# Kernel tuning notes

Measured on AMD Instinct MI355X. Metric: run time of the kernel, lower is better.

The kernel has to match this reference:

```python
import jax, jax.numpy as jnp
import numpy as np

N = 10000
E = 80000


def gat_layer(x, src, dst, W, a_src, a_dst, b):
    # x: [N, Fin], W: [Fin, Fout]
    xw = x @ W                              # [N, Fout]
    al_src = xw @ a_src                     # [N]
    al_dst = xw @ a_dst                     # [N]
    e = jax.nn.leaky_relu(al_src[src] + al_dst[dst], 0.2)  # [E+N]
    m = jax.lax.stop_gradient(jax.ops.segment_max(e, dst, num_segments=N))
    ex = jnp.exp(e - m[dst])
    denom = jax.ops.segment_sum(ex, dst, num_segments=N)
    alpha = ex / (denom[dst] + 1e-16)       # PyG softmax eps
    out = jax.ops.segment_sum(alpha[:, None] * xw[src], dst, num_segments=N)
    return out + b


def setup_inputs() -> dict:
    key = jax.random.key(0)
    ks = jax.random.split(key, 12)
    x = jax.random.normal(ks[0], (N, 256), dtype=jnp.float32)
    edge_index = jax.random.randint(ks[1], (2, E), 0, N, dtype=jnp.int64)
    def glorot(k, fi, fo):
        return jax.random.normal(k, (fi, fo), jnp.float32) * jnp.sqrt(2.0 / (fi + fo))
    W1 = glorot(ks[2], 256, 2048)
    W2 = glorot(ks[3], 2048, 2048)
    W3 = glorot(ks[4], 2048, 1024)
    a1s = jax.random.normal(ks[5], (2048,), jnp.float32) * 0.05
    a1d = jax.random.normal(ks[6], (2048,), jnp.float32) * 0.05
    a2s = jax.random.normal(ks[7], (2048,), jnp.float32) * 0.05
    a2d = jax.random.normal(ks[8], (2048,), jnp.float32) * 0.05
    a3s = jax.random.normal(ks[9], (1024,), jnp.float32) * 0.05
    a3d = jax.random.normal(ks[10], (1024,), jnp.float32) * 0.05
    b1 = jnp.zeros((2048,), jnp.float32)
    b2 = jnp.zeros((2048,), jnp.float32)
    b3 = jnp.zeros((1024,), jnp.float32)
    return {"x": x, "edge_index": edge_index, "W1": W1, "W2": W2, "W3": W3,
            "a1s": a1s, "a1d": a1d, "a2s": a2s, "a2d": a2d, "a3s": a3s, "a3d": a3d,
            "b1": b1, "b2": b2, "b3": b3}


def reference(x, edge_index, W1, W2, W3, a1s, a1d, a2s, a2d, a3s, a3d, b1, b2, b3):
    # add self loops (PyG GATConv default add_self_loops=True)
    loop = jnp.arange(N, dtype=edge_index.dtype)
    src = jnp.concatenate([edge_index[0], loop])
    dst = jnp.concatenate([edge_index[1], loop])
    h = jax.nn.relu(gat_layer(x, src, dst, W1, a1s, a1d, b1))
    h = jax.nn.relu(gat_layer(h, src, dst, W2, a2s, a2d, b2))
    h = jax.nn.relu(gat_layer(h, src, dst, W3, a3s, a3d, b3))
    # F.normalize(dim=1), eps=1e-12
    norm = jnp.linalg.norm(h, axis=1, keepdims=True)
    return h / jnp.maximum(norm, 1e-12)
```

## Files before the change

kernel.cpp:

```cpp
#include <hip/hip_runtime.h>
#include <hip/hip_bf16.h>
#include <math.h>


typedef __attribute__((ext_vector_type(8))) short short8;
typedef __attribute__((ext_vector_type(4))) float f32x4;

#define GLOAD_LDS16(g, l)                                            \
  __builtin_amdgcn_global_load_lds(                                  \
      (const __attribute__((address_space(1))) void*)(g),            \
      (__attribute__((address_space(3))) void*)(l), 16, 0, 0)

__device__ __forceinline__ float bf16_to_f32(ushort u) {
  return __uint_as_float(((unsigned int)u) << 16);
}

__device__ __forceinline__ float block_reduce_sum_bcast(float v) {
#pragma unroll
  for (int off = 32; off > 0; off >>= 1) v += __shfl_down(v, off, 64);
  __shared__ float tmp[4];
  __shared__ float res;
  int lane = threadIdx.x & 63, w = threadIdx.x >> 6;
  if (lane == 0) tmp[w] = v;
  __syncthreads();
  if (threadIdx.x == 0) res = tmp[0] + tmp[1] + tmp[2] + tmp[3];
  __syncthreads();
  float out = res;
  __syncthreads();
  return out;
}

__device__ __forceinline__ float block_reduce_max_bcast(float v) {
#pragma unroll
  for (int off = 32; off > 0; off >>= 1) v = fmaxf(v, __shfl_down(v, off, 64));
  __shared__ float tmpm[4];
  __shared__ float resm;
  int lane = threadIdx.x & 63, w = threadIdx.x >> 6;
  if (lane == 0) tmpm[w] = v;
  __syncthreads();
  if (threadIdx.x == 0) resm = fmaxf(fmaxf(tmpm[0], tmpm[1]), fmaxf(tmpm[2], tmpm[3]));
  __syncthreads();
  float out = resm;
  __syncthreads();
  return out;
}

__global__ void detect_kernel(const int* __restrict__ ei32, int* __restrict__ flag) {
  __shared__ int cnt;
  if (threadIdx.x == 0) cnt = 0;
  __syncthreads();
  int zeros = 0;
  for (int i = threadIdx.x; i < 1024; i += 256) {
    if (ei32[2 * i + 1] == 0) zeros++;
  }
  atomicAdd(&cnt, zeros);
  __syncthreads();
  if (threadIdx.x == 0) *flag = (cnt > 900) ? 1 : 0;
}

__global__ void convert_kernel(const void* __restrict__ ei, const int* __restrict__ flag,
                               int E, int* __restrict__ src, int* __restrict__ dst) {
  int i = blockIdx.x * blockDim.x + threadIdx.x;
  if (i >= E) return;
  if (*flag) {
    const long long* p = (const long long*)ei;
    src[i] = (int)p[i];
    dst[i] = (int)p[E + i];
  } else {
    const int* p = (const int*)ei;
    src[i] = p[i];
    dst[i] = p[E + i];
  }
}

__global__ __launch_bounds__(256) void convert_f32_bf16(const float* __restrict__ in,
                                                        __hip_bfloat16* __restrict__ out,
                                                        int n) {
  int i = blockIdx.x * blockDim.x + threadIdx.x;
  if (i < n) out[i] = __float2bfloat16(in[i]);
}

__global__ __launch_bounds__(256) void transpose_w(const float* __restrict__ W,
                                                   __hip_bfloat16* __restrict__ Wt,
                                                   int K, int Nout) {
  __shared__ float t[32][33];
  int tx = threadIdx.x & 31, ty = threadIdx.x >> 5;
  int n0 = blockIdx.x * 32, k0 = blockIdx.y * 32;
#pragma unroll
  for (int i = 0; i < 4; ++i) {
    int k = k0 + ty + i * 8;
    t[ty + i * 8][tx] = W[(size_t)k * Nout + n0 + tx];
  }
  __syncthreads();
#pragma unroll
  for (int i = 0; i < 4; ++i) {
    int n = n0 + ty + i * 8;
    Wt[(size_t)n * K + k0 + tx] = __float2bfloat16(t[tx][ty + i * 8]);
  }
}

template <bool BF16OUT>
__global__ __launch_bounds__(512, 2) void gemm256(const ushort* __restrict__ A,
                                                  const ushort* __restrict__ Bt,
                                                  void* __restrict__ C,
                                                  int M, int K, int Nout) {
  extern __shared__ ushort lds[];
  const int tid = threadIdx.x;
  const int l = tid & 63, w = tid >> 6;
  const int wm = w >> 2, wn = w & 3;
  const int l15 = l & 15, lhi = l >> 4;
  const int row0 = blockIdx.y * 256, col0 = blockIdx.x * 256;
  const int c8sw = (l & 3) ^ (((l >> 5) & 1) << 1);
  const int lrow = l >> 2;
  const int chsw = lhi ^ (((l15 >> 3) & 1) << 1);
  const int rd_off = l15 * 32 + chsw * 8;

  const ushort* ga[2][2];
  const ushort* gb[2][2];
  const int sA0 = wm * 8 + wn * 2;
  const int sB0 = (wn >> 1) * 8 + (wm * 2 + (wn & 1)) * 2;
#pragma unroll
  for (int sc = 0; sc < 2; ++sc) {
#pragma unroll
    for (int j = 0; j < 2; ++j) {
      int ar = min(row0 + (sA0 + j) * 16 + lrow, M - 1);
      ga[sc][j] = A + (size_t)ar * K + sc * 32 + c8sw * 8;
      gb[sc][j] = Bt + (size_t)(col0 + (sB0 + j) * 16 + lrow) * K + sc * 32 + c8sw * 8;
    }
  }

#define STAGE_A(nb, kn, sc)                                                       \
  do {                                                                            \
    GLOAD_LDS16(ga[sc][0] + (kn), &lds[(nb)*32768 + ((sA0 + 0) * 2 + (sc)) * 512]); \
    GLOAD_LDS16(ga[sc][1] + (kn), &lds[(nb)*32768 + ((sA0 + 1) * 2 + (sc)) * 512]); \
  } while (0)
#define STAGE_B(nb, kn, sc)                                                       \
  do {                                                                            \
    GLOAD_LDS16(gb[sc][0] + (kn), &lds[(nb)*32768 + 16384 + ((sB0 + 0) * 2 + (sc)) * 512]); \
    GLOAD_LDS16(gb[sc][1] + (kn), &lds[(nb)*32768 + 16384 + ((sB0 + 1) * 2 + (sc)) * 512]); \
  } while (0)

  f32x4 acc[8][4] = {};

#define PHASE(cur, mh, kk, STAGE_STMT)                                            \
  do {                                                                            \
    short8 af[4], bf[4];                                                          \
    const ushort* Ab = &lds[(cur)*32768];                                         \
    const ushort* Bb = &lds[(cur)*32768 + 16384];                                 \
    _Pragma("unroll") for (int m = 0; m < 4; ++m)                                 \
        af[m] = *(const short8*)(Ab + ((wm * 8 + (mh)*4 + m) * 2 + (kk)) * 512 + rd_off); \
    _Pragma("unroll") for (int n = 0; n < 4; ++n)                                 \
        bf[n] = *(const short8*)(Bb + ((wn * 4 + n) * 2 + (kk)) * 512 + rd_off);  \
    STAGE_STMT;                                                                   \
    asm volatile("s_waitcnt vmcnt(4)" ::: "memory");                              \
    __builtin_amdgcn_s_barrier();                                                 \
    __builtin_amdgcn_s_setprio(1);                                                \
    _Pragma("unroll") for (int m = 0; m < 4; ++m)                                 \
        _Pragma("unroll") for (int n = 0; n < 4; ++n)                             \
            acc[(mh)*4 + m][n] = __builtin_amdgcn_mfma_f32_16x16x32_bf16(         \
                af[m], bf[n], acc[(mh)*4 + m][n], 0, 0, 0);                       \
    __builtin_amdgcn_s_setprio(0);                                                \
    __builtin_amdgcn_s_barrier();                                                 \
  } while (0)

  STAGE_A(0, 0, 0);
  STAGE_B(0, 0, 0);
  STAGE_A(0, 0, 1);
  STAGE_B(0, 0, 1);
  asm volatile("s_waitcnt vmcnt(0)" ::: "memory");
  __builtin_amdgcn_s_barrier();

  const int nt = K >> 6;
  int cur = 0;
  for (int t = 0; t < nt; ++t) {
    const int kn = (t + 1) << 6;
    const bool pf = (t + 1) < nt;
    const int nb = cur ^ 1;
    PHASE(cur, 0, 0, if (pf) STAGE_A(nb, kn, 0));
    PHASE(cur, 1, 0, if (pf) STAGE_B(nb, kn, 0));
    PHASE(cur, 0, 1, if (pf) STAGE_A(nb, kn, 1));
    PHASE(cur, 1, 1, if (pf) STAGE_B(nb, kn, 1));
    cur ^= 1;
  }

#pragma unroll
  for (int mi = 0; mi < 8; ++mi) {
#pragma unroll
    for (int v = 0; v < 4; ++v) {
      int r = row0 + wm * 128 + mi * 16 + lhi * 4 + v;
      if (r < M) {
#pragma unroll
        for (int n = 0; n < 4; ++n) {
          size_t idx = (size_t)r * Nout + col0 + wn * 64 + n * 16 + l15;
          if (BF16OUT)
            ((__hip_bfloat16*)C)[idx] = __float2bfloat16(acc[mi][n][v]);
          else
            ((float*)C)[idx] = acc[mi][n][v];
        }
      }
    }
  }
#undef PHASE
#undef STAGE_A
#undef STAGE_B
}

template <bool BF16IN>
__global__ __launch_bounds__(256) void compute_al(const void* __restrict__ xw,
                                                  const float* __restrict__ a_s,
                                                  const float* __restrict__ a_d,
                                                  float* __restrict__ als,
                                                  float* __restrict__ ald, int F) {
  int n = blockIdx.x;
  float s1 = 0.f, s2 = 0.f;
  if (BF16IN) {
    const ushort* row = (const ushort*)xw + (size_t)n * F;
    int base = threadIdx.x * 8;
    short8 v = *(const short8*)(row + base);
#pragma unroll
    for (int j = 0; j < 8; ++j) {
      float f = bf16_to_f32((ushort)v[j]);
      s1 += f * a_s[base + j];
      s2 += f * a_d[base + j];
    }
  } else {
    const float* row = (const float*)xw + (size_t)n * F;
    for (int f = threadIdx.x; f < F; f += 256) {
      float v = row[f];
      s1 += v * a_s[f];
      s2 += v * a_d[f];
    }
  }
  float r1 = block_reduce_sum_bcast(s1);
  float r2 = block_reduce_sum_bcast(s2);
  if (threadIdx.x == 0) {
    als[n] = r1;
    ald[n] = r2;
  }
}

__global__ void count_kernel(const int* __restrict__ dst, int* __restrict__ counts, int E) {
  int i = blockIdx.x * blockDim.x + threadIdx.x;
  if (i < E) atomicAdd(&counts[dst[i]], 1);
}

__global__ __launch_bounds__(1024) void scan_kernel(const int* __restrict__ counts,
                                                    int* __restrict__ rowptr,
                                                    int* __restrict__ cursor, int Nn) {
  __shared__ int part[1024];
  int tid = threadIdx.x;
  int chunk = (Nn + 1023) / 1024;
  int base = tid * chunk;
  int s = 0;
  for (int i = 0; i < chunk; ++i) {
    int idx = base + i;
    if (idx < Nn) s += counts[idx];
  }
  part[tid] = s;
  __syncthreads();
  for (int off = 1; off < 1024; off <<= 1) {
    int v = 0;
    if (tid >= off) v = part[tid - off];
    __syncthreads();
    if (tid >= off) part[tid] += v;
    __syncthreads();
  }
  int run = (tid == 0) ? 0 : part[tid - 1];
  for (int i = 0; i < chunk; ++i) {
    int idx = base + i;
    if (idx < Nn) {
      rowptr[idx] = run;
      cursor[idx] = run;
      run += counts[idx];
    }
  }
  if (tid == 1023) rowptr[Nn] = part[1023];
}

__global__ void fill_kernel(const int* __restrict__ src, const int* __restrict__ dst,
                            int* __restrict__ cursor, int* __restrict__ eidx, int E) {
  int i = blockIdx.x * blockDim.x + threadIdx.x;
  if (i < E) {
    int pos = atomicAdd(&cursor[dst[i]], 1);
    eidx[pos] = src[i];
  }
}

template <int FPT, bool BF16IN, bool BF16OUT>
__global__ __launch_bounds__(256) void aggregate(const void* __restrict__ xw,
                                                 const float* __restrict__ als,
                                                 const float* __restrict__ ald,
                                                 const int* __restrict__ rowptr,
                                                 const int* __restrict__ eidx,
                                                 const float* __restrict__ bias,
                                                 void* __restrict__ out, int F) {
  int n = blockIdx.x;
  int tid = threadIdx.x;
  int beg = rowptr[n], end = rowptr[n + 1];
  int deg = end - beg;
  float aldn = ald[n];

  float lm = -INFINITY;
  for (int j = tid; j < deg; j += 256) {
    int s = eidx[beg + j];
    float e = als[s] + aldn;
    e = (e > 0.f) ? e : 0.2f * e;
    lm = fmaxf(lm, e);
  }
  if (tid == 0) {
    float e = als[n] + aldn;
    e = (e > 0.f) ? e : 0.2f * e;
    lm = fmaxf(lm, e);
  }
  float m = block_reduce_max_bcast(lm);

  float ls = 0.f;
  for (int j = tid; j < deg; j += 256) {
    int s = eidx[beg + j];
    float e = als[s] + aldn;
    e = (e > 0.f) ? e : 0.2f * e;
    ls += expf(e - m);
  }
  if (tid == 0) {
    float e = als[n] + aldn;
    e = (e > 0.f) ? e : 0.2f * e;
    ls += expf(e - m);
  }
  float denom = block_reduce_sum_bcast(ls) + 1e-16f;
  float inv_denom = 1.f / denom;

  float acc[FPT];
#pragma unroll
  for (int i = 0; i < FPT; ++i) acc[i] = 0.f;

  __shared__ float alpha_sh[256];
  __shared__ int src_sh[256];
  int total = deg + 1;
  for (int c0 = 0; c0 < total; c0 += 256) {
    int j = c0 + tid;
    if (j < total) {
      int s = (j < deg) ? eidx[beg + j] : n;
      float e = als[s] + aldn;
      e = (e > 0.f) ? e : 0.2f * e;
      alpha_sh[tid] = expf(e - m) * inv_denom;
      src_sh[tid] = s;
    }
    __syncthreads();
    int cn = min(256, total - c0);
    for (int jj = 0; jj < cn; ++jj) {
      float al = alpha_sh[jj];
      if (BF16IN) {
        const ushort* row = (const ushort*)xw + (size_t)src_sh[jj] * F;
#pragma unroll
        for (int i = 0; i < FPT / 2; ++i) {
          unsigned int u = *(const unsigned int*)(row + tid * 2 + i * 512);
          acc[2 * i]     += al * __uint_as_float((u & 0xffffu) << 16);
          acc[2 * i + 1] += al * __uint_as_float(u & 0xffff0000u);
        }
      } else {
        const float* row = (const float*)xw + (size_t)src_sh[jj] * F;
#pragma unroll
        for (int i = 0; i < FPT; ++i) acc[i] += al * row[tid + i * 256];
      }
    }
    __syncthreads();
  }

#pragma unroll
  for (int i = 0; i < FPT; ++i) {
    int col = BF16IN ? (tid * 2 + (i >> 1) * 512 + (i & 1)) : (tid + i * 256);
    float v = fmaxf(acc[i] + bias[col], 0.f);
    size_t idx = (size_t)n * F + col;
    if (BF16OUT)
      ((__hip_bfloat16*)out)[idx] = __float2bfloat16(v);
    else
      ((float*)out)[idx] = v;
  }
}

__global__ __launch_bounds__(256) void normalize_kernel(const float* __restrict__ h,
                                                        float* __restrict__ out,
                                                        int F) {
  int n = blockIdx.x;
  const float* row = h + (size_t)n * F;
  float ss = 0.f;
  for (int f = threadIdx.x; f < F; f += 256) {
    float v = row[f];
    ss += v * v;
  }
  float tot = block_reduce_sum_bcast(ss);
  float inv = 1.f / fmaxf(sqrtf(tot), 1e-12f);
  for (int f = threadIdx.x; f < F; f += 256) {
    out[(size_t)n * F + f] = row[f] * inv;
  }
}

extern "C" void kernel_launch(void* const* d_in, const int* in_sizes, int n_in,
                              void* d_out, int out_size, void* d_ws, size_t ws_size,
                              hipStream_t stream) {
  const float* x   = (const float*)d_in[0];
  const void*  ei  = d_in[1];
  const float* W1  = (const float*)d_in[2];
  const float* W2  = (const float*)d_in[3];
  const float* W3  = (const float*)d_in[4];
  const float* a1s = (const float*)d_in[5];
  const float* a1d = (const float*)d_in[6];
  const float* a2s = (const float*)d_in[7];
  const float* a2d = (const float*)d_in[8];
  const float* a3s = (const float*)d_in[9];
  const float* a3d = (const float*)d_in[10];
  const float* b1  = (const float*)d_in[11];
  const float* b2  = (const float*)d_in[12];
  const float* b3  = (const float*)d_in[13];

  const int N = in_sizes[0] / 256;
  const int E = in_sizes[1] / 2;

  char* ws = (char*)d_ws;
  size_t off = 0;
  auto alloc = [&](size_t bytes) -> void* {
    void* p = ws + off;
    off += (bytes + 255) & ~(size_t)255;
    return p;
  };
  ushort* xwb = (ushort*)alloc((size_t)N * 2048 * 2);
  ushort* hbf = (ushort*)alloc((size_t)N * 2048 * 2);
  float* bufA = (float*)alloc((size_t)N * 1024 * 4);
  __hip_bfloat16* xb  = (__hip_bfloat16*)alloc((size_t)N * 256 * 2);
  __hip_bfloat16* Wt1 = (__hip_bfloat16*)alloc((size_t)2048 * 256 * 2);
  __hip_bfloat16* Wt2 = (__hip_bfloat16*)alloc((size_t)2048 * 2048 * 2);
  __hip_bfloat16* Wt3 = (__hip_bfloat16*)alloc((size_t)1024 * 2048 * 2);
  float* als   = (float*)alloc((size_t)N * 4);
  float* ald   = (float*)alloc((size_t)N * 4);
  int* counts  = (int*)alloc((size_t)N * 4);
  int* rowptr  = (int*)alloc((size_t)(N + 1) * 4);
  int* cursor  = (int*)alloc((size_t)N * 4);
  int* eidx    = (int*)alloc((size_t)E * 4);
  int* src32   = (int*)alloc((size_t)E * 4);
  int* dst32   = (int*)alloc((size_t)E * 4);
  int* flag    = (int*)alloc(256);

  static bool attr_done = false;
  if (!attr_done) {
    hipFuncSetAttribute((const void*)gemm256<true>,
                        hipFuncAttributeMaxDynamicSharedMemorySize, 131072);
    hipFuncSetAttribute((const void*)gemm256<false>,
                        hipFuncAttributeMaxDynamicSharedMemorySize, 131072);
    attr_done = true;
  }

  detect_kernel<<<1, 256, 0, stream>>>((const int*)ei, flag);
  convert_kernel<<<(E + 255) / 256, 256, 0, stream>>>(ei, flag, E, src32, dst32);
  hipMemsetAsync(counts, 0, (size_t)N * 4, stream);
  count_kernel<<<(E + 255) / 256, 256, 0, stream>>>(dst32, counts, E);
  scan_kernel<<<1, 1024, 0, stream>>>(counts, rowptr, cursor, N);
  fill_kernel<<<(E + 255) / 256, 256, 0, stream>>>(src32, dst32, cursor, eidx, E);

  convert_f32_bf16<<<(N * 256 + 255) / 256, 256, 0, stream>>>(x, xb, N * 256);
  transpose_w<<<dim3(2048 / 32, 256 / 32), 256, 0, stream>>>(W1, Wt1, 256, 2048);
  transpose_w<<<dim3(2048 / 32, 2048 / 32), 256, 0, stream>>>(W2, Wt2, 2048, 2048);
  transpose_w<<<dim3(1024 / 32, 2048 / 32), 256, 0, stream>>>(W3, Wt3, 2048, 1024);

  dim3 blk(256);
  dim3 gblk(512);
  int mb = (N + 255) / 256;

  gemm256<true><<<dim3(2048 / 256, mb), gblk, 131072, stream>>>((const ushort*)xb, (const ushort*)Wt1, xwb, N, 256, 2048);
  compute_al<true><<<N, blk, 0, stream>>>(xwb, a1s, a1d, als, ald, 2048);
  aggregate<8, true, true><<<N, blk, 0, stream>>>(xwb, als, ald, rowptr, eidx, b1, hbf, 2048);

  gemm256<true><<<dim3(2048 / 256, mb), gblk, 131072, stream>>>(hbf, (const ushort*)Wt2, xwb, N, 2048, 2048);
  compute_al<true><<<N, blk, 0, stream>>>(xwb, a2s, a2d, als, ald, 2048);
  aggregate<8, true, true><<<N, blk, 0, stream>>>(xwb, als, ald, rowptr, eidx, b2, hbf, 2048);

  gemm256<false><<<dim3(1024 / 256, mb), gblk, 131072, stream>>>(hbf, (const ushort*)Wt3, bufA, N, 2048, 1024);
  compute_al<false><<<N, blk, 0, stream>>>(bufA, a3s, a3d, als, ald, 1024);
  float* hf32 = (float*)xwb;
  aggregate<4, false, false><<<N, blk, 0, stream>>>(bufA, als, ald, rowptr, eidx, b3, hf32, 1024);

  normalize_kernel<<<N, blk, 0, stream>>>(hf32, (float*)d_out, 1024);
}
```

Measured before the change: 474.6 us.

## Shrink GEMM tile to 256x128, triple-buffer LDS, and swizzle block order

The GEMM tile changes from 256x256 to 256x128 output columns. This doubles the grid so more of the 256 CUs are busy, since 40 row blocks times 8 column blocks underfills the device. LDS moves from double to triple buffering with a prefetch distance of two K-steps. Block indices are remapped across groups of 8 to improve L2 locality. The trade-off is lower arithmetic intensity per block, and 144KB of LDS likely limits occupancy to one block per CU.

```diff
diff --git a/kernel.cpp b/kernel.cpp
--- a/kernel.cpp
+++ b/kernel.cpp
@@ -100,87 +100,87 @@
 }
 
 template <bool BF16OUT>
-__global__ __launch_bounds__(512, 2) void gemm256(const ushort* __restrict__ A,
-                                                  const ushort* __restrict__ Bt,
-                                                  void* __restrict__ C,
-                                                  int M, int K, int Nout) {
+__global__ __launch_bounds__(512, 2) void gemm_bn128(const ushort* __restrict__ A,
+                                                     const ushort* __restrict__ Bt,
+                                                     void* __restrict__ C,
+                                                     int M, int K, int Nout) {
+  constexpr int BUF = 16384 + 8192;
   extern __shared__ ushort lds[];
   const int tid = threadIdx.x;
   const int l = tid & 63, w = tid >> 6;
   const int wm = w >> 2, wn = w & 3;
   const int l15 = l & 15, lhi = l >> 4;
-  const int row0 = blockIdx.y * 256, col0 = blockIdx.x * 256;
+
+  int nwg = gridDim.x * gridDim.y;
+  int lin = blockIdx.y * gridDim.x + blockIdx.x;
+  if ((nwg & 7) == 0) lin = (lin & 7) * (nwg >> 3) + (lin >> 3);
+  const int bx = lin % gridDim.x, by = lin / gridDim.x;
+  const int row0 = by * 256, col0 = bx * 128;
+
   const int c8sw = (l & 3) ^ (((l >> 5) & 1) << 1);
   const int lrow = l >> 2;
   const int chsw = lhi ^ (((l15 >> 3) & 1) << 1);
   const int rd_off = l15 * 32 + chsw * 8;
 
+  const int sA0 = wm * 8 + wn * 2;
+  const int sB0 = w;
   const ushort* ga[2][2];
-  const ushort* gb[2][2];
-  const int sA0 = wm * 8 + wn * 2;
-  const int sB0 = (wn >> 1) * 8 + (wm * 2 + (wn & 1)) * 2;
+  const ushort* gb[2];
 #pragma unroll
   for (int sc = 0; sc < 2; ++sc) {
 #pragma unroll
     for (int j = 0; j < 2; ++j) {
       int ar = min(row0 + (sA0 + j) * 16 + lrow, M - 1);
       ga[sc][j] = A + (size_t)ar * K + sc * 32 + c8sw * 8;
-      gb[sc][j] = Bt + (size_t)(col0 + (sB0 + j) * 16 + lrow) * K + sc * 32 + c8sw * 8;
-    }
-  }
-
-#define STAGE_A(nb, kn, sc)                                                       \
-  do {                                                                            \
-    GLOAD_LDS16(ga[sc][0] + (kn), &lds[(nb)*32768 + ((sA0 + 0) * 2 + (sc)) * 512]); \
-    GLOAD_LDS16(ga[sc][1] + (kn), &lds[(nb)*32768 + ((sA0 + 1) * 2 + (sc)) * 512]); \
+    }
+    gb[sc] = Bt + (size_t)(col0 + sB0 * 16 + lrow) * K + sc * 32 + c8sw * 8;
+  }
+
+#define STAGE_PH(nb, kn, sc)                                                         \
+  do {                                                                               \
+    GLOAD_LDS16(ga[sc][0] + (kn), &lds[(nb)*BUF + ((sA0 + 0) * 2 + (sc)) * 512]);    \
+    GLOAD_LDS16(ga[sc][1] + (kn), &lds[(nb)*BUF + ((sA0 + 1) * 2 + (sc)) * 512]);    \
+    GLOAD_LDS16(gb[sc] + (kn), &lds[(nb)*BUF + 16384 + (sB0 * 2 + (sc)) * 512]);     \
   } while (0)
-#define STAGE_B(nb, kn, sc)                                                       \
-  do {                                                                            \
-    GLOAD_LDS16(gb[sc][0] + (kn), &lds[(nb)*32768 + 16384 + ((sB0 + 0) * 2 + (sc)) * 512]); \
-    GLOAD_LDS16(gb[sc][1] + (kn), &lds[(nb)*32768 + 16384 + ((sB0 + 1) * 2 + (sc)) * 512]); \
+
+  f32x4 acc[8][2] = {};
+
+#define PHASE(cbase, kk, STAGE_STMT)                                                 \
+  do {                                                                               \
+    short8 af[8], bf[2];                                                             \
+    _Pragma("unroll") for (int m = 0; m < 8; ++m)                                    \
+        af[m] = *(const short8*)(cbase + ((wm * 8 + m) * 2 + (kk)) * 512 + rd_off);  \
+    _Pragma("unroll") for (int n = 0; n < 2; ++n)                                    \
+        bf[n] = *(const short8*)(cbase + 16384 + ((wn * 2 + n) * 2 + (kk)) * 512 + rd_off); \
+    STAGE_STMT;                                                                      \
+    asm volatile("s_waitcnt vmcnt(6)" ::: "memory");                                 \
+    __builtin_amdgcn_s_barrier();                                                    \
+    __builtin_amdgcn_s_setprio(1);                                                   \
+    _Pragma("unroll") for (int m = 0; m < 8; ++m)                                    \
+        _Pragma("unroll") for (int n = 0; n < 2; ++n)                                \
+            acc[m][n] = __builtin_amdgcn_mfma_f32_16x16x32_bf16(                     \
+                af[m], bf[n], acc[m][n], 0, 0, 0);                                   \
+    __builtin_amdgcn_s_setprio(0);                                                   \
+    __builtin_amdgcn_s_barrier();                                                    \
   } while (0)
 
-  f32x4 acc[8][4] = {};
-
-#define PHASE(cur, mh, kk, STAGE_STMT)                                            \
-  do {                                                                            \
-    short8 af[4], bf[4];                                                          \
-    const ushort* Ab = &lds[(cur)*32768];                                         \
-    const ushort* Bb = &lds[(cur)*32768 + 16384];                                 \
-    _Pragma("unroll") for (int m = 0; m < 4; ++m)                                 \
-        af[m] = *(const short8*)(Ab + ((wm * 8 + (mh)*4 + m) * 2 + (kk)) * 512 + rd_off); \
-    _Pragma("unroll") for (int n = 0; n < 4; ++n)                                 \
-        bf[n] = *(const short8*)(Bb + ((wn * 4 + n) * 2 + (kk)) * 512 + rd_off);  \
-    STAGE_STMT;                                                                   \
-    asm volatile("s_waitcnt vmcnt(4)" ::: "memory");                              \
-    __builtin_amdgcn_s_barrier();                                                 \
-    __builtin_amdgcn_s_setprio(1);                                                \
-    _Pragma("unroll") for (int m = 0; m < 4; ++m)                                 \
-        _Pragma("unroll") for (int n = 0; n < 4; ++n)                             \
-            acc[(mh)*4 + m][n] = __builtin_amdgcn_mfma_f32_16x16x32_bf16(         \
-                af[m], bf[n], acc[(mh)*4 + m][n], 0, 0, 0);                       \
-    __builtin_amdgcn_s_setprio(0);                                                \
-    __builtin_amdgcn_s_barrier();                                                 \
-  } while (0)
-
-  STAGE_A(0, 0, 0);
-  STAGE_B(0, 0, 0);
-  STAGE_A(0, 0, 1);
-  STAGE_B(0, 0, 1);
-  asm volatile("s_waitcnt vmcnt(0)" ::: "memory");
+  const int nt = K >> 6;
+  STAGE_PH(0, 0, 0);
+  STAGE_PH(0, 0, 1);
+  STAGE_PH(1, 64, 0);
+  STAGE_PH(1, 64, 1);
+  asm volatile("s_waitcnt vmcnt(6)" ::: "memory");
   __builtin_amdgcn_s_barrier();
 
-  const int nt = K >> 6;
   int cur = 0;
   for (int t = 0; t < nt; ++t) {
-    const int kn = (t + 1) << 6;
-    const bool pf = (t + 1) < nt;
-    const int nb = cur ^ 1;
-    PHASE(cur, 0, 0, if (pf) STAGE_A(nb, kn, 0));
-    PHASE(cur, 1, 0, if (pf) STAGE_B(nb, kn, 0));
-    PHASE(cur, 0, 1, if (pf) STAGE_A(nb, kn, 1));
-    PHASE(cur, 1, 1, if (pf) STAGE_B(nb, kn, 1));
-    cur ^= 1;
+    const ushort* cb = &lds[cur * BUF];
+    int nb = cur + 2; if (nb >= 3) nb -= 3;
+    const bool pf = (t + 2) < nt;
+    const int kn = (t + 2) << 6;
+    PHASE(cb, 0, if (pf) STAGE_PH(nb, kn, 0));
+    PHASE(cb, 1, if (pf) STAGE_PH(nb, kn, 1));
+    cur = cur + 1; if (cur == 3) cur = 0;
   }
 
 #pragma unroll
@@ -190,8 +190,8 @@
       int r = row0 + wm * 128 + mi * 16 + lhi * 4 + v;
       if (r < M) {
 #pragma unroll
-        for (int n = 0; n < 4; ++n) {
-          size_t idx = (size_t)r * Nout + col0 + wn * 64 + n * 16 + l15;
+        for (int n = 0; n < 2; ++n) {
+          size_t idx = (size_t)r * Nout + col0 + wn * 32 + n * 16 + l15;
           if (BF16OUT)
             ((__hip_bfloat16*)C)[idx] = __float2bfloat16(acc[mi][n][v]);
           else
@@ -201,8 +201,7 @@
     }
   }
 #undef PHASE
-#undef STAGE_A
-#undef STAGE_B
+#undef STAGE_PH
 }
 
 template <bool BF16IN>
@@ -442,10 +441,10 @@
 
   static bool attr_done = false;
   if (!attr_done) {
-    hipFuncSetAttribute((const void*)gemm256<true>,
-                        hipFuncAttributeMaxDynamicSharedMemorySize, 131072);
-    hipFuncSetAttribute((const void*)gemm256<false>,
-                        hipFuncAttributeMaxDynamicSharedMemorySize, 131072);
+    hipFuncSetAttribute((const void*)gemm_bn128<true>,
+                        hipFuncAttributeMaxDynamicSharedMemorySize, 147456);
+    hipFuncSetAttribute((const void*)gemm_bn128<false>,
+                        hipFuncAttributeMaxDynamicSharedMemorySize, 147456);
     attr_done = true;
   }
 
@@ -465,15 +464,15 @@
   dim3 gblk(512);
   int mb = (N + 255) / 256;
 
-  gemm256<true><<<dim3(2048 / 256, mb), gblk, 131072, stream>>>((const ushort*)xb, (const ushort*)Wt1, xwb, N, 256, 2048);
+  gemm_bn128<true><<<dim3(2048 / 128, mb), gblk, 147456, stream>>>((const ushort*)xb, (const ushort*)Wt1, xwb, N, 256, 2048);
   compute_al<true><<<N, blk, 0, stream>>>(xwb, a1s, a1d, als, ald, 2048);
   aggregate<8, true, true><<<N, blk, 0, stream>>>(xwb, als, ald, rowptr, eidx, b1, hbf, 2048);
 
-  gemm256<true><<<dim3(2048 / 256, mb), gblk, 131072, stream>>>(hbf, (const ushort*)Wt2, xwb, N, 2048, 2048);
+  gemm_bn128<true><<<dim3(2048 / 128, mb), gblk, 147456, stream>>>(hbf, (const ushort*)Wt2, xwb, N, 2048, 2048);
   compute_al<true><<<N, blk, 0, stream>>>(xwb, a2s, a2d, als, ald, 2048);
   aggregate<8, true, true><<<N, blk, 0, stream>>>(xwb, als, ald, rowptr, eidx, b2, hbf, 2048);
 
-  gemm256<false><<<dim3(1024 / 256, mb), gblk, 131072, stream>>>(hbf, (const ushort*)Wt3, bufA, N, 2048, 1024);
+  gemm_bn128<false><<<dim3(1024 / 128, mb), gblk, 147456, stream>>>(hbf, (const ushort*)Wt3, bufA, N, 2048, 1024);
   compute_al<false><<<N, blk, 0, stream>>>(bufA, a3s, a3d, als, ald, 1024);
   float* hf32 = (float*)xwb;
   aggregate<4, false, false><<<N, blk, 0, stream>>>(bufA, als, ald, rowptr, eidx, b3, hf32, 1024);
```

Result: no change. 465.3 us (-2.0%).
